# Performance work log

Hardware: AMD Instinct MI355X
Metric: run time of the kernel (lower is better)

The kernel has to match this reference:

```python
import jax, jax.numpy as jnp
import numpy as np

N, K, D = 65536, 1024, 512
ALPHA = 1.0

def setup_inputs() -> dict:
    key = jax.random.key(0)
    k1, k2 = jax.random.split(key)
    batch = jax.random.normal(k1, (N, D), dtype=jnp.float32)
    # Xavier uniform init for cluster centers: bound = sqrt(6/(K+D))
    bound = float(np.sqrt(6.0 / (K + D)))
    cluster_centers = jax.random.uniform(k2, (K, D), dtype=jnp.float32, minval=-bound, maxval=bound)
    return {"batch": batch, "cluster_centers": cluster_centers}

def reference(batch, cluster_centers):
    x_sq = jnp.sum(batch * batch, axis=1, keepdims=True)            # [N,1]
    c_sq = jnp.sum(cluster_centers * cluster_centers, axis=1)       # [K]
    cross = batch @ cluster_centers.T                               # [N,K]
    norm_squared = jnp.maximum(x_sq - 2.0 * cross + c_sq[None, :], 0.0)
    numerator = 1.0 / (1.0 + norm_squared / ALPHA)
    power = (ALPHA + 1.0) / 2.0
    numerator = numerator ** power
    return numerator / jnp.sum(numerator, axis=1, keepdims=True)
```

## Files before the change

kernel.cpp:

```cpp
#include <hip/hip_runtime.h>
#include <hip/hip_bf16.h>
#include <stdint.h>


#define N_ROWS 65536
#define K_CL   1024
#define D_DIM  512
#define BM     64

typedef __attribute__((ext_vector_type(8))) short short8;
typedef __attribute__((ext_vector_type(4))) float f32x4;

__device__ __forceinline__ ushort f2bf(float f) {
    union { float f; uint32_t u; } v; v.f = f;
    uint32_t u = v.u;
    u += 0x7fffu + ((u >> 16) & 1u);
    return (ushort)(u >> 16);
}

__device__ __forceinline__ float waveReduceSum(float s) {
#pragma unroll
    for (int off = 32; off; off >>= 1) s += __shfl_down(s, off, 64);
    return s;
}

__global__ void prep_rows(const float* __restrict__ X, ushort* __restrict__ Xbf,
                          float* __restrict__ sq) {
    const int row  = blockIdx.x * 4 + (threadIdx.x >> 6);
    const int lane = threadIdx.x & 63;
    const float4* src = (const float4*)(X + (size_t)row * D_DIM);
    float4 a = src[lane * 2];
    float4 b = src[lane * 2 + 1];
    float s = (a.x*a.x + a.y*a.y) + (a.z*a.z + a.w*a.w)
            + (b.x*b.x + b.y*b.y) + (b.z*b.z + b.w*b.w);
    uint4 o;
    o.x = (uint32_t)f2bf(a.x) | ((uint32_t)f2bf(a.y) << 16);
    o.y = (uint32_t)f2bf(a.z) | ((uint32_t)f2bf(a.w) << 16);
    o.z = (uint32_t)f2bf(b.x) | ((uint32_t)f2bf(b.y) << 16);
    o.w = (uint32_t)f2bf(b.z) | ((uint32_t)f2bf(b.w) << 16);
    *(uint4*)(Xbf + (size_t)row * D_DIM + lane * 8) = o;
    s = waveReduceSum(s);
    if (lane == 0) sq[row] = s;
}

__global__ __launch_bounds__(512, 2) void gemm_fused(
    const ushort* __restrict__ A, const ushort* __restrict__ B,
    const float* __restrict__ xsq, const float* __restrict__ csq,
    float* __restrict__ out)
{
    __shared__ __align__(16) ushort smA[BM * D_DIM];

    const int tid  = threadIdx.x;
    const int w    = tid >> 6;
    const int lane = tid & 63;
    const int l4 = lane >> 4, l16 = lane & 15;
    const int rbase = blockIdx.x * BM;

#pragma unroll
    for (int i = 0; i < 8; ++i) {
        const int row = i * 8 + w;
        const int sl  = lane ^ (row & 15);
        __builtin_amdgcn_global_load_lds(
            (const __attribute__((address_space(1))) void*)
                (A + (size_t)(rbase + row) * D_DIM + sl * 8),
            (__attribute__((address_space(3))) void*)(smA + (size_t)row * D_DIM),
            16, 0, 0);
    }

    const ushort* gB[8];
#pragma unroll
    for (int n = 0; n < 8; ++n)
        gB[n] = B + (size_t)(w * 128 + n * 16 + l16) * D_DIM + l4 * 8;

    f32x4 acc[4][8] = {};

    __syncthreads();

#pragma unroll 2
    for (int t = 0; t < 16; ++t) {
        short8 bf[8];
#pragma unroll
        for (int n = 0; n < 8; ++n)
            bf[n] = *(const short8*)(gB[n] + t * 32);
        short8 af[4];
#pragma unroll
        for (int m = 0; m < 4; ++m) {
            const int row = m * 16 + l16;
            af[m] = *(const short8*)((const char*)smA
                    + row * 1024 + (((t * 4 + l4) ^ l16) << 4));
        }
#pragma unroll
        for (int m = 0; m < 4; ++m)
#pragma unroll
            for (int n = 0; n < 8; ++n)
                acc[m][n] = __builtin_amdgcn_mfma_f32_16x16x32_bf16(
                    af[m], bf[n], acc[m][n], 0, 0, 0);
    }

    float xs[4][4];
#pragma unroll
    for (int m = 0; m < 4; ++m)
#pragma unroll
        for (int r = 0; r < 4; ++r)
            xs[m][r] = xsq[rbase + m * 16 + l4 * 4 + r];

    float s[4][4] = {{0.f}};
#pragma unroll
    for (int n = 0; n < 8; ++n) {
        const float cs = csq[w * 128 + n * 16 + l16];
#pragma unroll
        for (int m = 0; m < 4; ++m)
#pragma unroll
            for (int r = 0; r < 4; ++r) {
                float ns = fmaxf(xs[m][r] - 2.0f * acc[m][n][r] + cs, 0.0f);
                float p = 1.0f / (1.0f + ns);
                acc[m][n][r] = p;
                s[m][r] += p;
            }
    }
#pragma unroll
    for (int m = 0; m < 4; ++m)
#pragma unroll
        for (int r = 0; r < 4; ++r) {
            float v = s[m][r];
            v += __shfl_xor(v, 1, 64);
            v += __shfl_xor(v, 2, 64);
            v += __shfl_xor(v, 4, 64);
            v += __shfl_xor(v, 8, 64);
            s[m][r] = v;
        }

    __syncthreads();
    float* smRS  = (float*)smA;
    float* smInv = (float*)smA + 512;
    if (l16 == 0) {
#pragma unroll
        for (int m = 0; m < 4; ++m)
#pragma unroll
            for (int r = 0; r < 4; ++r)
                smRS[w * 64 + m * 16 + l4 * 4 + r] = s[m][r];
    }
    __syncthreads();
    if (tid < 64) {
        float t = 0.f;
#pragma unroll
        for (int j = 0; j < 8; ++j) t += smRS[j * 64 + tid];
        smInv[tid] = 1.0f / t;
    }
    __syncthreads();

    float inv[4][4];
#pragma unroll
    for (int m = 0; m < 4; ++m)
#pragma unroll
        for (int r = 0; r < 4; ++r)
            inv[m][r] = smInv[m * 16 + l4 * 4 + r];

#pragma unroll
    for (int m = 0; m < 4; ++m)
#pragma unroll
        for (int n = 0; n < 8; ++n) {
            const int col = w * 128 + n * 16 + l16;
#pragma unroll
            for (int r = 0; r < 4; ++r) {
                const int row = rbase + m * 16 + l4 * 4 + r;
                out[(size_t)row * K_CL + col] = acc[m][n][r] * inv[m][r];
            }
        }
}

extern "C" void kernel_launch(void* const* d_in, const int* in_sizes, int n_in,
                              void* d_out, int out_size, void* d_ws, size_t ws_size,
                              hipStream_t stream) {
    const float* batch   = (const float*)d_in[0];
    const float* centers = (const float*)d_in[1];
    float* out = (float*)d_out;

    char* ws = (char*)d_ws;
    ushort* Abf = (ushort*)ws;
    ushort* Bbf = (ushort*)(ws + (size_t)N_ROWS * D_DIM * 2);
    float*  xsq = (float*)(ws + (size_t)N_ROWS * D_DIM * 2
                              + (size_t)K_CL * D_DIM * 2);
    float*  csq = xsq + N_ROWS;
    (void)in_sizes; (void)n_in; (void)out_size; (void)ws_size;

    prep_rows<<<K_CL / 4,   256, 0, stream>>>(centers, Bbf, csq);
    prep_rows<<<N_ROWS / 4, 256, 0, stream>>>(batch, Abf, xsq);
    gemm_fused<<<N_ROWS / BM, 512, 0, stream>>>(Abf, Bbf, xsq, csq, out);
}
```

Measured before the change: 240.9 us.

## Make GEMM persistent with double-buffered LDS pipeline for A and B tiles

Replaces the one-tile-per-block GEMM with a persistent grid of 256 blocks. Each block walks 4 row tiles and streams K-slices of both A and B through double-buffered LDS using async global_load_lds, with explicit vmcnt waits and barriers. This is meant to overlap global loads with MFMA work and to stop reading B fragments directly from global memory. It also raises wave priority around the MFMA block. The trade-offs are a barrier every K-step, a larger LDS footprint, and the epilogue now running inside the main loop, where it stalls the pipeline.

```diff
diff --git a/kernel.cpp b/kernel.cpp
--- a/kernel.cpp
+++ b/kernel.cpp
@@ -6,10 +6,11 @@
 #define N_ROWS 65536
 #define K_CL   1024
 #define D_DIM  512
-#define BM     64
 
 typedef __attribute__((ext_vector_type(8))) short short8;
 typedef __attribute__((ext_vector_type(4))) float f32x4;
+
+#define SCHED0() __builtin_amdgcn_sched_barrier(0)
 
 __device__ __forceinline__ ushort f2bf(float f) {
     union { float f; uint32_t u; } v; v.f = f;
@@ -48,125 +49,155 @@
     const float* __restrict__ xsq, const float* __restrict__ csq,
     float* __restrict__ out)
 {
-    __shared__ __align__(16) ushort smA[BM * D_DIM];
+    __shared__ __align__(16) ushort smA[2][2048];
+    __shared__ __align__(16) ushort smB[8][2][4096];
+    __shared__ float smR[576];
 
     const int tid  = threadIdx.x;
     const int w    = tid >> 6;
     const int lane = tid & 63;
     const int l4 = lane >> 4, l16 = lane & 15;
-    const int rbase = blockIdx.x * BM;
-
-#pragma unroll
-    for (int i = 0; i < 8; ++i) {
-        const int row = i * 8 + w;
-        const int sl  = lane ^ (row & 15);
-        __builtin_amdgcn_global_load_lds(
-            (const __attribute__((address_space(1))) void*)
-                (A + (size_t)(rbase + row) * D_DIM + sl * 8),
-            (__attribute__((address_space(3))) void*)(smA + (size_t)row * D_DIM),
-            16, 0, 0);
-    }
-
-    const ushort* gB[8];
-#pragma unroll
-    for (int n = 0; n < 8; ++n)
-        gB[n] = B + (size_t)(w * 128 + n * 16 + l16) * D_DIM + l4 * 8;
+    const int bid = blockIdx.x;
+
+    const uint arow  = (uint)((tid & 255) >> 2);
+    const uint aslot = (uint)((tid & 3) ^ ((tid >> 3) & 3)) * 8u;
+    const uint boffc = (uint)(w * 128 + (lane >> 2)) * 512u
+                     + (uint)((lane & 3) ^ ((lane >> 3) & 3)) * 8u;
+
+    const int swz = ((l16 >> 1) & 3) << 4;
+    int aoff[4], boff[8];
+#pragma unroll
+    for (int m = 0; m < 4; ++m) aoff[m] = (m*16 + l16)*64 + ((l4*16) ^ swz);
+#pragma unroll
+    for (int n = 0; n < 8; ++n) boff[n] = (n*16 + l16)*64 + ((l4*16) ^ swz);
 
     f32x4 acc[4][8] = {};
 
-    __syncthreads();
-
-#pragma unroll 2
-    for (int t = 0; t < 16; ++t) {
-        short8 bf[8];
-#pragma unroll
-        for (int n = 0; n < 8; ++n)
-            bf[n] = *(const short8*)(gB[n] + t * 32);
-        short8 af[4];
-#pragma unroll
-        for (int m = 0; m < 4; ++m) {
-            const int row = m * 16 + l16;
-            af[m] = *(const short8*)((const char*)smA
-                    + row * 1024 + (((t * 4 + l4) ^ l16) << 4));
+#define STAGE_GRP(H) do {                                                    \
+        const int  _sl = (H) & 1;                                            \
+        const uint _k0 = (uint)(((H) & 15) * 32);                            \
+        const uint _pr = (uint)(bid + 256 * ((H) >> 4)) * 64u;               \
+        __builtin_amdgcn_global_load_lds(                                    \
+            (const __attribute__((address_space(1))) void*)                  \
+                (A + (size_t)(_pr + arow) * 512u + _k0 + aslot),             \
+            (__attribute__((address_space(3))) void*)(&smA[_sl][(w & 3) * 512]), \
+            16, 0, 0);                                                       \
+        _Pragma("unroll")                                                    \
+        for (int _i = 0; _i < 8; ++_i)                                       \
+            __builtin_amdgcn_global_load_lds(                                \
+                (const __attribute__((address_space(1))) void*)              \
+                    (B + (size_t)boffc + (size_t)_i * 8192u + _k0),          \
+                (__attribute__((address_space(3))) void*)(&smB[w][_sl][_i * 512]), \
+                16, 0, 0);                                                   \
+    } while (0)
+
+#define LBAR() do { asm volatile("s_waitcnt lgkmcnt(0)" ::: "memory");       \
+        SCHED0(); __builtin_amdgcn_s_barrier(); SCHED0(); } while (0)
+
+    STAGE_GRP(0);
+
+    for (int G = 0; G < 64; ++G) {
+        SCHED0(); __builtin_amdgcn_s_barrier(); SCHED0();
+        if (G < 63) {
+            STAGE_GRP(G + 1);
+            asm volatile("s_waitcnt vmcnt(9)" ::: "memory");
+        } else {
+            asm volatile("s_waitcnt vmcnt(0)" ::: "memory");
         }
+        SCHED0(); __builtin_amdgcn_s_barrier(); SCHED0();
+
+        const int sl = G & 1;
+        const char* bA = (const char*)&smA[sl][0];
+        const char* bB = (const char*)&smB[w][sl][0];
+        short8 af[4], bf[8];
+#pragma unroll
+        for (int m = 0; m < 4; ++m) af[m] = *(const short8*)(bA + aoff[m]);
+#pragma unroll
+        for (int n = 0; n < 8; ++n) bf[n] = *(const short8*)(bB + boff[n]);
+
+        __builtin_amdgcn_s_setprio(1);
 #pragma unroll
         for (int m = 0; m < 4; ++m)
 #pragma unroll
             for (int n = 0; n < 8; ++n)
                 acc[m][n] = __builtin_amdgcn_mfma_f32_16x16x32_bf16(
                     af[m], bf[n], acc[m][n], 0, 0, 0);
+        __builtin_amdgcn_s_setprio(0);
+
+        if ((G & 15) == 15) {
+            const size_t prow0 = (size_t)(bid + 256 * (G >> 4)) * 64u;
+            float xs[4][4];
+#pragma unroll
+            for (int m = 0; m < 4; ++m)
+#pragma unroll
+                for (int r = 0; r < 4; ++r)
+                    xs[m][r] = xsq[prow0 + m*16 + l4*4 + r];
+
+            float s[4][4] = {{0.f}};
+#pragma unroll
+            for (int n = 0; n < 8; ++n) {
+                const float cs = csq[w*128 + n*16 + l16];
+#pragma unroll
+                for (int m = 0; m < 4; ++m)
+#pragma unroll
+                    for (int r = 0; r < 4; ++r) {
+                        float ns = fmaxf(xs[m][r] - 2.0f*acc[m][n][r] + cs, 0.0f);
+                        float p = 1.0f / (1.0f + ns);
+                        acc[m][n][r] = p;
+                        s[m][r] += p;
+                    }
+            }
+#pragma unroll
+            for (int m = 0; m < 4; ++m)
+#pragma unroll
+                for (int r = 0; r < 4; ++r) {
+                    float v = s[m][r];
+                    v += __shfl_xor(v, 1, 64);
+                    v += __shfl_xor(v, 2, 64);
+                    v += __shfl_xor(v, 4, 64);
+                    v += __shfl_xor(v, 8, 64);
+                    s[m][r] = v;
+                }
+            if (l16 == 0) {
+#pragma unroll
+                for (int m = 0; m < 4; ++m)
+#pragma unroll
+                    for (int r = 0; r < 4; ++r)
+                        smR[w*64 + m*16 + l4*4 + r] = s[m][r];
+            }
+            LBAR();
+            if (tid < 64) {
+                float t = 0.f;
+#pragma unroll
+                for (int j = 0; j < 8; ++j) t += smR[j*64 + tid];
+                smR[512 + tid] = 1.0f / t;
+            }
+            LBAR();
+            float inv[4][4];
+#pragma unroll
+            for (int m = 0; m < 4; ++m)
+#pragma unroll
+                for (int r = 0; r < 4; ++r)
+                    inv[m][r] = smR[512 + m*16 + l4*4 + r];
+#pragma unroll
+            for (int m = 0; m < 4; ++m)
+#pragma unroll
+                for (int n = 0; n < 8; ++n) {
+                    const int col = w*128 + n*16 + l16;
+#pragma unroll
+                    for (int r = 0; r < 4; ++r)
+                        out[(prow0 + m*16 + l4*4 + r) * K_CL + col]
+                            = acc[m][n][r] * inv[m][r];
+                }
+#pragma unroll
+            for (int m = 0; m < 4; ++m)
+#pragma unroll
+                for (int n = 0; n < 8; ++n)
+                    acc[m][n] = (f32x4){0.f, 0.f, 0.f, 0.f};
+        }
     }
-
-    float xs[4][4];
-#pragma unroll
-    for (int m = 0; m < 4; ++m)
-#pragma unroll
-        for (int r = 0; r < 4; ++r)
-            xs[m][r] = xsq[rbase + m * 16 + l4 * 4 + r];
-
-    float s[4][4] = {{0.f}};
-#pragma unroll
-    for (int n = 0; n < 8; ++n) {
-        const float cs = csq[w * 128 + n * 16 + l16];
-#pragma unroll
-        for (int m = 0; m < 4; ++m)
-#pragma unroll
-            for (int r = 0; r < 4; ++r) {
-                float ns = fmaxf(xs[m][r] - 2.0f * acc[m][n][r] + cs, 0.0f);
-                float p = 1.0f / (1.0f + ns);
-                acc[m][n][r] = p;
-                s[m][r] += p;
-            }
-    }
-#pragma unroll
-    for (int m = 0; m < 4; ++m)
-#pragma unroll
-        for (int r = 0; r < 4; ++r) {
-            float v = s[m][r];
-            v += __shfl_xor(v, 1, 64);
-            v += __shfl_xor(v, 2, 64);
-            v += __shfl_xor(v, 4, 64);
-            v += __shfl_xor(v, 8, 64);
-            s[m][r] = v;
-        }
-
-    __syncthreads();
-    float* smRS  = (float*)smA;
-    float* smInv = (float*)smA + 512;
-    if (l16 == 0) {
-#pragma unroll
-        for (int m = 0; m < 4; ++m)
-#pragma unroll
-            for (int r = 0; r < 4; ++r)
-                smRS[w * 64 + m * 16 + l4 * 4 + r] = s[m][r];
-    }
-    __syncthreads();
-    if (tid < 64) {
-        float t = 0.f;
-#pragma unroll
-        for (int j = 0; j < 8; ++j) t += smRS[j * 64 + tid];
-        smInv[tid] = 1.0f / t;
-    }
-    __syncthreads();
-
-    float inv[4][4];
-#pragma unroll
-    for (int m = 0; m < 4; ++m)
-#pragma unroll
-        for (int r = 0; r < 4; ++r)
-            inv[m][r] = smInv[m * 16 + l4 * 4 + r];
-
-#pragma unroll
-    for (int m = 0; m < 4; ++m)
-#pragma unroll
-        for (int n = 0; n < 8; ++n) {
-            const int col = w * 128 + n * 16 + l16;
-#pragma unroll
-            for (int r = 0; r < 4; ++r) {
-                const int row = rbase + m * 16 + l4 * 4 + r;
-                out[(size_t)row * K_CL + col] = acc[m][n][r] * inv[m][r];
-            }
-        }
+#undef STAGE_GRP
+#undef LBAR
 }
 
 extern "C" void kernel_launch(void* const* d_in, const int* in_sizes, int n_in,
@@ -186,5 +217,5 @@
 
     prep_rows<<<K_CL / 4,   256, 0, stream>>>(centers, Bbf, csq);
     prep_rows<<<N_ROWS / 4, 256, 0, stream>>>(batch, Abf, xsq);
-    gemm_fused<<<N_ROWS / BM, 512, 0, stream>>>(Abf, Bbf, xsq, csq, out);
-}
+    gemm_fused<<<256, 512, 0, stream>>>(Abf, Bbf, xsq, csq, out);
+}
```

Result: faster. 231.6 us (-3.9%).
